# Optimization experiments

Hardware: AMD Instinct MI355X
Metric: run time of the kernel (lower is better)

## Reference

```python
import jax, jax.numpy as jnp
import numpy as np

T_VID = 129  # TACoS iou grid size

def make_iou_mask_map():
    m = np.zeros((129, 129), np.float32)
    for i in range(0, 128):
        m[i, 1 + i:min(i + 17, 129)] = 1.0
    for i in range(0, 128 - 16, 2):
        m[i, list(range(18 + i, min(33 + i, 129), 2))] = 1.0
    for i in range(0, 128 - 32, 4):
        m[i, list(range(36 + i, min(65 + i, 129), 4))] = 1.0
    for i in range(0, 128 - 64, 8):
        m[i, list(range(72 + i, 129, 8))] = 1.0
    return jnp.asarray(m)

def setup_inputs() -> dict:
    key = jax.random.key(0)
    B, L, T, D, CH, V = 8, 100, T_VID, 512, 512, 1000
    ks = jax.random.split(key, 20)
    g = lambda k, shp, fan: jax.random.normal(k, shp, jnp.float32) * (1.0 / np.sqrt(fan))
    return {
        'hidden_states_text': jax.random.normal(ks[0], (B, L, D), jnp.float32),
        'hidden_states_object': jax.random.normal(ks[1], (B, T, D), jnp.float32),
        # final_mlp (text head): D->CH->V
        'w_t1': g(ks[2], (D, CH), D), 'b_t1': jnp.zeros((CH,), jnp.float32),
        'w_t2': g(ks[3], (CH, V), CH), 'b_t2': jnp.zeros((V,), jnp.float32),
        # final_mlp_2: D -> 3D (+ReLU)
        'w2': g(ks[4], (D, 3 * D), D), 'b2': jnp.zeros((3 * D,), jnp.float32),
        # final_mlp_3: 3D -> CH -> 3
        'w3a': g(ks[5], (3 * D, CH), 3 * D), 'b3a': jnp.zeros((CH,), jnp.float32),
        'w3b': g(ks[6], (CH, 3), CH), 'b3b': jnp.zeros((3,), jnp.float32),
        # final_mlp_s/e/c: D -> CH -> 1
        'w_s1': g(ks[7], (D, CH), D), 'b_s1': jnp.zeros((CH,), jnp.float32),
        'w_s2': g(ks[8], (CH, 1), CH), 'b_s2': jnp.zeros((1,), jnp.float32),
        'w_e1': g(ks[9], (D, CH), D), 'b_e1': jnp.zeros((CH,), jnp.float32),
        'w_e2': g(ks[10], (CH, 1), CH), 'b_e2': jnp.zeros((1,), jnp.float32),
        'w_c1': g(ks[11], (D, CH), D), 'b_c1': jnp.zeros((CH,), jnp.float32),
        'w_c2': g(ks[12], (CH, 1), CH), 'b_c2': jnp.zeros((1,), jnp.float32),
    }

def _head(x, w1, b1, w2, b2):
    return jax.nn.relu(x @ w1 + b1) @ w2 + b2

def reference(hidden_states_text, hidden_states_object,
              w_t1, b_t1, w_t2, b_t2, w2, b2, w3a, b3a, w3b, b3b,
              w_s1, b_s1, w_s2, b_s2, w_e1, b_e1, w_e2, b_e2,
              w_c1, b_c1, w_c2, b_c2):
    D = hidden_states_object.shape[-1]
    T = hidden_states_object.shape[1]
    # text head (dropout is identity at inference)
    logits_text = _head(hidden_states_text, w_t1, b_t1, w_t2, b_t2)
    # final_mlp_2 then split into start/center/end streams, each [B,T,D]
    h = jax.nn.relu(hidden_states_object @ w2 + b2)
    hs, hc, he = h[..., :D], h[..., D:2 * D], h[..., 2 * D:]
    # final_mlp_3 first linear decomposed over the concat blocks:
    # grid[b,i,j] = W_s.hs[i] + W_c.hc[(i+j)//2] + W_e.he[j] + b  (same math as
    # cat(repeat(hs), gather(hc), repeat(he)) @ w3a, without the 3D grid)
    ps = hc @ w3a[D:2 * D]            # [B,T,CH] (center projection, gathered below)
    pS = hs @ w3a[:D]                 # [B,T,CH]
    pE = he @ w3a[2 * D:]             # [B,T,CH]
    idx = (jnp.arange(T)[:, None] + jnp.arange(T)[None, :]) // 2  # [T,T] center index
    grid = pS[:, :, None, :] + ps[:, idx, :] + pE[:, None, :, :] + b3a  # [B,T,T,CH]
    logits_iou = (jax.nn.relu(grid) @ w3b + b3b)  # [B,T,T,3]
    logits_iou = jnp.transpose(logits_iou, (0, 3, 1, 2))  # [B,3,T,T]
    logits_visual = jnp.concatenate([
        _head(hs, w_s1, b_s1, w_s2, b_s2),
        _head(he, w_e1, b_e1, w_e2, b_e2),
        _head(hc, w_c1, b_c1, w_c2, b_c2)], axis=-1)  # [B,T,3]
    return logits_text, logits_visual, logits_iou, make_iou_mask_map()
```

## Files before the change

### kernel.cpp

```cpp
#include <hip/hip_runtime.h>
#include <hip/hip_bf16.h>

typedef unsigned short ushort_t;
typedef __attribute__((ext_vector_type(8))) short bf16x8;
typedef __attribute__((ext_vector_type(4))) float f32x4;

constexpr int BB = 8, LL = 100, TT = 129, DD = 512, CH = 512, VV = 1000;
constexpr int M_TXT = BB * LL;
constexpr int M_OBJ = BB * TT;
constexpr int P_SLAB = M_OBJ * DD;
constexpr int N_IOU = BB * 3 * TT * TT;
constexpr int N_VIS = 3 * M_OBJ;
constexpr int N_MASK = TT * TT;

constexpr int OUT_TEXT = 0;
constexpr int OUT_VIS  = M_TXT * VV;
constexpr int OUT_IOU  = OUT_VIS + N_VIS;
constexpr int OUT_MASK = OUT_IOU + N_IOU;

constexpr size_t WB_TEXT = 0;
constexpr size_t WB_OBJ  = WB_TEXT + 819200;
constexpr size_t WB_WT1  = WB_OBJ  + 1056768;
constexpr size_t WB_WT2  = WB_WT1  + 524288;
constexpr size_t WB_W2T  = WB_WT2  + 1024000;
constexpr size_t WB_W3AT = WB_W2T  + 1572864;
constexpr size_t WB_WS1T = WB_W3AT + 1572864;
constexpr size_t WB_WE1T = WB_WS1T + 524288;
constexpr size_t WB_WC1T = WB_WE1T + 524288;
constexpr size_t WB_T1   = WB_WC1T + 524288;
constexpr size_t WB_H    = WB_T1   + 819200;
constexpr size_t WB_P    = WB_H    + 3170304;

__device__ __forceinline__ ushort_t f2bf(float x) {
    __hip_bfloat16 h = __float2bfloat16(x);
    return *(ushort_t*)&h;
}

struct TDesc { const float* src; ushort_t* dst; int R, C, tiles, ctiles; };
struct PrepArgs {
    const float* act_a; ushort_t* act_da; int na4;
    const float* act_b; ushort_t* act_db; int nb4;
    int nact_blocks, nwt_blocks;
    TDesc t[7];
    const float *b3b, *bs2, *be2, *bc2;
    float* out;
};

__global__ __launch_bounds__(256)
void prep_kernel(PrepArgs pa)
{
    const int bxg = blockIdx.x;
    if (bxg < pa.nact_blocks) {
        int gid = bxg * 256 + threadIdx.x;
        const float* src; ushort_t* dst;
        if (gid < pa.na4) { src = pa.act_a + gid * 4; dst = pa.act_da + gid * 4; }
        else { gid -= pa.na4; if (gid >= pa.nb4) return; src = pa.act_b + gid * 4; dst = pa.act_db + gid * 4; }
        f32x4 v = *(const f32x4*)src;
        dst[0] = f2bf(v[0]); dst[1] = f2bf(v[1]); dst[2] = f2bf(v[2]); dst[3] = f2bf(v[3]);
        return;
    }
    if (bxg < pa.nact_blocks + pa.nwt_blocks) {
        __shared__ float tl[32][33];
        int bx = bxg - pa.nact_blocks;
        TDesc e;
        #pragma unroll
        for (int i = 0; i < 7; ++i) {
            if (bx < pa.t[i].tiles) { e = pa.t[i]; break; }
            bx -= pa.t[i].tiles;
        }
        const int tx = threadIdx.x & 31, ty = threadIdx.x >> 5;
        const int rt = bx / e.ctiles, ct = bx - rt * e.ctiles;
        #pragma unroll
        for (int i = 0; i < 4; ++i) {
            const int r = rt * 32 + ty + i * 8, c = ct * 32 + tx;
            tl[ty + i * 8][tx] = (r < e.R && c < e.C) ? e.src[(size_t)r * e.C + c] : 0.0f;
        }
        __syncthreads();
        #pragma unroll
        for (int i = 0; i < 4; ++i) {
            const int dr = ct * 32 + ty + i * 8, dc = rt * 32 + tx;
            if (dr < e.C && dc < e.R)
                e.dst[(size_t)dr * e.R + dc] = f2bf(tl[tx][ty + i * 8]);
        }
        return;
    }
    int g = (bxg - pa.nact_blocks - pa.nwt_blocks) * 256 + threadIdx.x;
    if (g < N_IOU) {
        const int bk = g / (TT * TT);
        const int k = bk - (bk / 3) * 3;
        pa.out[OUT_IOU + g] = pa.b3b[k];
        return;
    }
    g -= N_IOU;
    if (g < N_VIS) {
        const int head = g - (g / 3) * 3;
        const float bias = head == 0 ? pa.bs2[0] : (head == 1 ? pa.be2[0] : pa.bc2[0]);
        pa.out[OUT_VIS + g] = bias;
        return;
    }
    g -= N_VIS;
    if (g < N_MASK) {
        const int i = g / TT, j = g - i * TT;
        const int d = j - i;
        bool v = false;
        if (i < 128 && d >= 1 && d <= 16) v = true;
        if (!v && (i & 1) == 0 && i <= 110 && d >= 18 && d <= 32 && (d & 1) == 0) v = true;
        if (!v && (i & 3) == 0 && i <= 92  && d >= 36 && d <= 64 && (d & 3) == 0) v = true;
        if (!v && (i & 7) == 0 && i <= 56  && d >= 72 && (d & 7) == 0) v = true;
        pa.out[OUT_MASK + g] = v ? 1.0f : 0.0f;
    }
}

struct GemmDesc {
    const ushort_t* A; int lda;
    const ushort_t* Bt; int ldb;
    const float* bias;
    void* C; int ldc;
    int M, N, K;
    int mode;
    const float* w2head;
    float* vbase;
    int vhead;
    int ntiles, ntx;
};
struct GemmArgs { GemmDesc d[7]; };

__global__ __launch_bounds__(256)
void gemm_mfma(GemmArgs args)
{
    int bx = blockIdx.x, zi = 0;
    while (bx >= args.d[zi].ntiles) { bx -= args.d[zi].ntiles; ++zi; }
    const GemmDesc g = args.d[zi];
    const int tyT = bx / g.ntx, txT = bx - tyT * g.ntx;
    const int m0 = tyT * 128, n0 = txT * 128;

    __shared__ ushort_t ldsA[2][128 * 32];
    __shared__ ushort_t ldsB[2][128 * 32];

    const int tid = threadIdx.x;
    const int w = tid >> 6, l = tid & 63;
    const int wr = w >> 1, wc = w & 1;

    const int srow = l >> 2;
    const int scol = (l & 3) << 3;
    const int wbase = w << 4;

    f32x4 acc[4][4];
    #pragma unroll
    for (int mi = 0; mi < 4; ++mi)
        #pragma unroll
        for (int ni = 0; ni < 4; ++ni)
            acc[mi][ni] = f32x4{0.f, 0.f, 0.f, 0.f};

    const int nk = g.K >> 5;

    auto stage = [&](int buf, int k0) {
        #pragma unroll
        for (int q = 0; q < 2; ++q) {
            int gm = m0 + (q << 6) + wbase + srow; if (gm >= g.M) gm = g.M - 1;
            __builtin_amdgcn_global_load_lds(
                (const __attribute__((address_space(1))) unsigned int*)(g.A + (size_t)gm * g.lda + k0 + scol),
                (__attribute__((address_space(3))) unsigned int*)&ldsA[buf][((q << 6) + wbase) * 32],
                16, 0, 0);
            int gn = n0 + (q << 6) + wbase + srow; if (gn >= g.N) gn = g.N - 1;
            __builtin_amdgcn_global_load_lds(
                (const __attribute__((address_space(1))) unsigned int*)(g.Bt + (size_t)gn * g.ldb + k0 + scol),
                (__attribute__((address_space(3))) unsigned int*)&ldsB[buf][((q << 6) + wbase) * 32],
                16, 0, 0);
        }
    };

    stage(0, 0);
    int cur = 0;
    const int fr = l & 15, kq = (l >> 4) << 3;

    for (int kt = 0; kt < nk; ++kt) {
        __syncthreads();
        if (kt + 1 < nk) stage(cur ^ 1, (kt + 1) << 5);
        bf16x8 av[4], bv[4];
        #pragma unroll
        for (int mi = 0; mi < 4; ++mi)
            av[mi] = *(const bf16x8*)&ldsA[cur][((wr << 6) + (mi << 4) + fr) * 32 + kq];
        #pragma unroll
        for (int ni = 0; ni < 4; ++ni)
            bv[ni] = *(const bf16x8*)&ldsB[cur][((wc << 6) + (ni << 4) + fr) * 32 + kq];
        #pragma unroll
        for (int mi = 0; mi < 4; ++mi)
            #pragma unroll
            for (int ni = 0; ni < 4; ++ni)
                acc[mi][ni] = __builtin_amdgcn_mfma_f32_16x16x32_bf16(av[mi], bv[ni], acc[mi][ni], 0, 0, 0);
        cur ^= 1;
    }

    const int rq = (l >> 4) << 2;
    if (g.mode == 2) {
        float s[4][4];
        #pragma unroll
        for (int mi = 0; mi < 4; ++mi)
            #pragma unroll
            for (int r = 0; r < 4; ++r) s[mi][r] = 0.f;
        #pragma unroll
        for (int ni = 0; ni < 4; ++ni) {
            const int col = n0 + (wc << 6) + (ni << 4) + fr;
            const float bb = g.bias[col];
            const float wv = g.w2head[col];
            #pragma unroll
            for (int mi = 0; mi < 4; ++mi)
                #pragma unroll
                for (int r = 0; r < 4; ++r) {
                    float v = fmaxf(acc[mi][ni][r] + bb, 0.f);
                    s[mi][r] = fmaf(v, wv, s[mi][r]);
                }
        }
        #pragma unroll
        for (int off = 1; off < 16; off <<= 1)
            #pragma unroll
            for (int mi = 0; mi < 4; ++mi)
                #pragma unroll
                for (int r = 0; r < 4; ++r)
                    s[mi][r] += __shfl_xor(s[mi][r], off);
        if (fr == 0) {
            #pragma unroll
            for (int mi = 0; mi < 4; ++mi)
                #pragma unroll
                for (int r = 0; r < 4; ++r) {
                    const int row = m0 + (wr << 6) + (mi << 4) + rq + r;
                    if (row < g.M) atomicAdd(&g.vbase[row * 3 + g.vhead], s[mi][r]);
                }
        }
    } else {
        #pragma unroll
        for (int ni = 0; ni < 4; ++ni) {
            const int col = n0 + (wc << 6) + (ni << 4) + fr;
            const float bb = (g.bias && col < g.N) ? g.bias[col] : 0.f;
            #pragma unroll
            for (int mi = 0; mi < 4; ++mi)
                #pragma unroll
                for (int r = 0; r < 4; ++r) {
                    const int row = m0 + (wr << 6) + (mi << 4) + rq + r;
                    if (row < g.M && col < g.N) {
                        float v = acc[mi][ni][r] + bb;
                        if (g.mode == 1) {
                            v = fmaxf(v, 0.f);
                            ((ushort_t*)g.C)[(size_t)row * g.ldc + col] = f2bf(v);
                        } else {
                            ((float*)g.C)[(size_t)row * g.ldc + col] = v;
                        }
                    }
                }
        }
    }
}

__global__ __launch_bounds__(256)
void iou_kernel(const float* __restrict__ P, const float* __restrict__ w3b,
                float* __restrict__ out)
{
    __shared__ __align__(16) float sP[96 * 132];
    __shared__ __align__(16) float sW[384];

    const int tid = threadIdx.x;
    const int b = blockIdx.z >> 2;
    const int cs = blockIdx.z & 3;
    const int c0 = cs << 7;
    const int i0 = blockIdx.y * 32, j0 = blockIdx.x * 32;
    const int idx0 = (i0 + j0) >> 1;
    const int par = (i0 + j0) & 1;

    for (int f = tid; f < 384; f += 256) {
        const int k = f >> 7, c = f & 127;
        sW[f] = w3b[(c0 + c) * 3 + k];
    }
    for (int f = tid; f < 3072; f += 256) {
        const int row = f >> 5;
        const int pos = (f & 31) << 2;
        const int a = row >> 5;
        const int r = row & 31;
        int rg = (a == 0) ? (i0 + r) : (a == 1) ? (idx0 + r) : (j0 + r);
        if (rg > 128) rg = 128;
        f32x4 v = *(const f32x4*)&P[(size_t)a * P_SLAB + ((size_t)(b * TT) + rg) * DD + c0 + pos];
        *(f32x4*)&sP[row * 132 + pos] = v;
    }
    __syncthreads();

    const int ii = tid >> 4, jj = tid & 15;
    const int o = ((ii + jj + par) >> 1) + 32;

    const float* rs0 = &sP[ii * 132];
    const float* rs1 = &sP[(ii + 16) * 132];
    const float* rp0 = &sP[o * 132];
    const float* rp1 = &sP[(o + 8) * 132];
    const float* rp2 = &sP[(o + 16) * 132];
    const float* re0 = &sP[(64 + jj) * 132];
    const float* re1 = &sP[(64 + jj + 16) * 132];

    const f32x4 z4 = {0.f, 0.f, 0.f, 0.f};
    f32x4 av00[3], av01[3], av10[3], av11[3];
    #pragma unroll
    for (int k = 0; k < 3; ++k) { av00[k] = z4; av01[k] = z4; av10[k] = z4; av11[k] = z4; }

    #pragma unroll 2
    for (int c = 0; c < 128; c += 4) {
        const f32x4 s0 = *(const f32x4*)&rs0[c];
        const f32x4 s1 = *(const f32x4*)&rs1[c];
        const f32x4 p0 = *(const f32x4*)&rp0[c];
        const f32x4 p1 = *(const f32x4*)&rp1[c];
        const f32x4 p2 = *(const f32x4*)&rp2[c];
        const f32x4 e0 = *(const f32x4*)&re0[c];
        const f32x4 e1 = *(const f32x4*)&re1[c];
        const f32x4 w0 = *(const f32x4*)&sW[c];
        const f32x4 w1 = *(const f32x4*)&sW[128 + c];
        const f32x4 w2 = *(const f32x4*)&sW[256 + c];

        const f32x4 t00 = s0 + e0, t01 = s0 + e1, t10 = s1 + e0, t11 = s1 + e1;
        const f32x4 v00 = __builtin_elementwise_max(t00 + p0, z4);
        const f32x4 v01 = __builtin_elementwise_max(t01 + p1, z4);
        const f32x4 v10 = __builtin_elementwise_max(t10 + p1, z4);
        const f32x4 v11 = __builtin_elementwise_max(t11 + p2, z4);

        av00[0] = __builtin_elementwise_fma(v00, w0, av00[0]);
        av00[1] = __builtin_elementwise_fma(v00, w1, av00[1]);
        av00[2] = __builtin_elementwise_fma(v00, w2, av00[2]);
        av01[0] = __builtin_elementwise_fma(v01, w0, av01[0]);
        av01[1] = __builtin_elementwise_fma(v01, w1, av01[1]);
        av01[2] = __builtin_elementwise_fma(v01, w2, av01[2]);
        av10[0] = __builtin_elementwise_fma(v10, w0, av10[0]);
        av10[1] = __builtin_elementwise_fma(v10, w1, av10[1]);
        av10[2] = __builtin_elementwise_fma(v10, w2, av10[2]);
        av11[0] = __builtin_elementwise_fma(v11, w0, av11[0]);
        av11[1] = __builtin_elementwise_fma(v11, w1, av11[1]);
        av11[2] = __builtin_elementwise_fma(v11, w2, av11[2]);
    }

    auto emit = [&](const f32x4* acc, int i, int j) {
        if (i <= 128 && j <= 128) {
            #pragma unroll
            for (int k = 0; k < 3; ++k) {
                const float s = acc[k][0] + acc[k][1] + acc[k][2] + acc[k][3];
                atomicAdd(&out[OUT_IOU + ((size_t)(b * 3 + k) * TT + i) * TT + j], s);
            }
        }
    };
    emit(av00, i0 + ii, j0 + jj);
    emit(av01, i0 + ii, j0 + jj + 16);
    emit(av10, i0 + ii + 16, j0 + jj);
    emit(av11, i0 + ii + 16, j0 + jj + 16);
}

extern "C" void kernel_launch(void* const* d_in, const int* in_sizes, int n_in,
                              void* d_out, int out_size, void* d_ws, size_t ws_size,
                              hipStream_t stream)
{
    const float* text = (const float*)d_in[0];
    const float* obj  = (const float*)d_in[1];
    const float* w_t1 = (const float*)d_in[2];
    const float* b_t1 = (const float*)d_in[3];
    const float* w_t2 = (const float*)d_in[4];
    const float* b_t2 = (const float*)d_in[5];
    const float* w2   = (const float*)d_in[6];
    const float* b2   = (const float*)d_in[7];
    const float* w3a  = (const float*)d_in[8];
    const float* b3a  = (const float*)d_in[9];
    const float* w3b  = (const float*)d_in[10];
    const float* b3b  = (const float*)d_in[11];
    const float* w_s1 = (const float*)d_in[12];
    const float* b_s1 = (const float*)d_in[13];
    const float* w_s2 = (const float*)d_in[14];
    const float* b_s2 = (const float*)d_in[15];
    const float* w_e1 = (const float*)d_in[16];
    const float* b_e1 = (const float*)d_in[17];
    const float* w_e2 = (const float*)d_in[18];
    const float* b_e2 = (const float*)d_in[19];
    const float* w_c1 = (const float*)d_in[20];
    const float* b_c1 = (const float*)d_in[21];
    const float* w_c2 = (const float*)d_in[22];
    const float* b_c2 = (const float*)d_in[23];

    float* out = (float*)d_out;
    char* ws = (char*)d_ws;
    ushort_t* text_bf = (ushort_t*)(ws + WB_TEXT);
    ushort_t* obj_bf  = (ushort_t*)(ws + WB_OBJ);
    ushort_t* wt1     = (ushort_t*)(ws + WB_WT1);
    ushort_t* wt2     = (ushort_t*)(ws + WB_WT2);
    ushort_t* w2t     = (ushort_t*)(ws + WB_W2T);
    ushort_t* w3at    = (ushort_t*)(ws + WB_W3AT);
    ushort_t* ws1t    = (ushort_t*)(ws + WB_WS1T);
    ushort_t* we1t    = (ushort_t*)(ws + WB_WE1T);
    ushort_t* wc1t    = (ushort_t*)(ws + WB_WC1T);
    ushort_t* T1      = (ushort_t*)(ws + WB_T1);
    ushort_t* H       = (ushort_t*)(ws + WB_H);
    float*    P       = (float*)(ws + WB_P);

    {
        PrepArgs pa;
        pa.act_a = text; pa.act_da = text_bf; pa.na4 = (M_TXT * DD) / 4;
        pa.act_b = obj;  pa.act_db = obj_bf;  pa.nb4 = (M_OBJ * DD) / 4;
        pa.nact_blocks = (pa.na4 + pa.nb4 + 255) / 256;
        pa.nwt_blocks = 3072;
        pa.t[0] = {w_t1, wt1, 512, 512, 256, 16};
        pa.t[1] = {w_t2, wt2, 512, 1000, 512, 32};
        pa.t[2] = {w2, w2t, 512, 1536, 768, 48};
        pa.t[3] = {w3a, w3at, 1536, 512, 768, 16};
        pa.t[4] = {w_s1, ws1t, 512, 512, 256, 16};
        pa.t[5] = {w_e1, we1t, 512, 512, 256, 16};
        pa.t[6] = {w_c1, wc1t, 512, 512, 256, 16};
        pa.b3b = b3b; pa.bs2 = b_s2; pa.be2 = b_e2; pa.bc2 = b_c2;
        pa.out = out;
        const int ninit = (N_IOU + N_VIS + N_MASK + 255) / 256;
        prep_kernel<<<dim3(pa.nact_blocks + pa.nwt_blocks + ninit), dim3(256), 0, stream>>>(pa);
    }
    {
        GemmArgs a{};
        a.d[0] = {text_bf, DD, wt1, DD, b_t1, T1, CH, M_TXT, CH, DD, 1, nullptr, nullptr, 0, 28, 4};
        a.d[1] = {obj_bf, DD, w2t, DD, b2, H, 3 * DD, M_OBJ, 3 * DD, DD, 1, nullptr, nullptr, 0, 108, 12};
        gemm_mfma<<<dim3(136), dim3(256), 0, stream>>>(a);
    }
    {
        GemmArgs a{};
        a.d[0] = {T1, CH, wt2, CH, b_t2, out + OUT_TEXT, VV, M_TXT, VV, CH, 0, nullptr, nullptr, 0, 56, 8};
        a.d[1] = {H + 0 * DD, 3 * DD, w3at + 0 * DD, 3 * DD, b3a, P + 0 * P_SLAB, DD, M_OBJ, DD, DD, 0, nullptr, nullptr, 0, 36, 4};
        a.d[2] = {H + 1 * DD, 3 * DD, w3at + 1 * DD, 3 * DD, nullptr, P + 1 * P_SLAB, DD, M_OBJ, DD, DD, 0, nullptr, nullptr, 0, 36, 4};
        a.d[3] = {H + 2 * DD, 3 * DD, w3at + 2 * DD, 3 * DD, nullptr, P + 2 * P_SLAB, DD, M_OBJ, DD, DD, 0, nullptr, nullptr, 0, 36, 4};
        a.d[4] = {H + 0 * DD, 3 * DD, ws1t, DD, b_s1, nullptr, 0, M_OBJ, CH, DD, 2, w_s2, out + OUT_VIS, 0, 36, 4};
        a.d[5] = {H + 2 * DD, 3 * DD, we1t, DD, b_e1, nullptr, 0, M_OBJ, CH, DD, 2, w_e2, out + OUT_VIS, 1, 36, 4};
        a.d[6] = {H + 1 * DD, 3 * DD, wc1t, DD, b_c1, nullptr, 0, M_OBJ, CH, DD, 2, w_c2, out + OUT_VIS, 2, 36, 4};
        gemm_mfma<<<dim3(272), dim3(256), 0, stream>>>(a);
    }
    iou_kernel<<<dim3(5, 5, 32), dim3(256), 0, stream>>>(P, w3b, out);
}
```

Baseline: 87.46 us.

## Vectorize transpose stores, deepen GEMM K-step to 64, halve IoU atomic splits

The weight-transpose path now writes four bf16 values per thread in one packed store instead of scattered scalar stores. The MFMA GEMM stages 64 K-elements per barrier, doubling LDS buffers, to halve the number of sync iterations. The IoU kernel makes each block loop over two 128-channel chunks, halving grid size and atomicAdd traffic at the cost of less parallelism and serialized loads. The transpose store assumes the column range is full 32-wide and aligned with no dc<R check, which could write out of bounds or drop the tail when R is not a multiple of 32.

Result: faster. 81.86 us (-6.4%).

```diff
diff --git a/kernel.cpp b/kernel.cpp
--- a/kernel.cpp
+++ b/kernel.cpp
@@ -2,6 +2,7 @@
 #include <hip/hip_bf16.h>
 
 typedef unsigned short ushort_t;
+typedef __attribute__((ext_vector_type(4))) unsigned short u16x4;
 typedef __attribute__((ext_vector_type(8))) short bf16x8;
 typedef __attribute__((ext_vector_type(4))) float f32x4;
 
@@ -68,7 +69,8 @@
             if (bx < pa.t[i].tiles) { e = pa.t[i]; break; }
             bx -= pa.t[i].tiles;
         }
-        const int tx = threadIdx.x & 31, ty = threadIdx.x >> 5;
+        const int t = threadIdx.x;
+        const int tx = t & 31, ty = t >> 5;
         const int rt = bx / e.ctiles, ct = bx - rt * e.ctiles;
         #pragma unroll
         for (int i = 0; i < 4; ++i) {
@@ -76,11 +78,13 @@
             tl[ty + i * 8][tx] = (r < e.R && c < e.C) ? e.src[(size_t)r * e.C + c] : 0.0f;
         }
         __syncthreads();
-        #pragma unroll
-        for (int i = 0; i < 4; ++i) {
-            const int dr = ct * 32 + ty + i * 8, dc = rt * 32 + tx;
-            if (dr < e.C && dc < e.R)
-                e.dst[(size_t)dr * e.R + dc] = f2bf(tl[tx][ty + i * 8]);
+        const int drl = t >> 3, dcl = (t & 7) << 2;
+        const int grow = ct * 32 + drl;
+        if (grow < e.C) {
+            u16x4 v;
+            #pragma unroll
+            for (int u = 0; u < 4; ++u) v[u] = f2bf(tl[dcl + u][drl]);
+            *(u16x4*)&e.dst[(size_t)grow * e.R + rt * 32 + dcl] = v;
         }
         return;
     }
@@ -134,8 +138,8 @@
     const int tyT = bx / g.ntx, txT = bx - tyT * g.ntx;
     const int m0 = tyT * 128, n0 = txT * 128;
 
-    __shared__ ushort_t ldsA[2][128 * 32];
-    __shared__ ushort_t ldsB[2][128 * 32];
+    __shared__ ushort_t ldsA[2][2][128 * 32];
+    __shared__ ushort_t ldsB[2][2][128 * 32];
 
     const int tid = threadIdx.x;
     const int w = tid >> 6, l = tid & 63;
@@ -152,21 +156,24 @@
         for (int ni = 0; ni < 4; ++ni)
             acc[mi][ni] = f32x4{0.f, 0.f, 0.f, 0.f};
 
-    const int nk = g.K >> 5;
+    const int nk = g.K >> 6;
 
     auto stage = [&](int buf, int k0) {
         #pragma unroll
-        for (int q = 0; q < 2; ++q) {
-            int gm = m0 + (q << 6) + wbase + srow; if (gm >= g.M) gm = g.M - 1;
-            __builtin_amdgcn_global_load_lds(
-                (const __attribute__((address_space(1))) unsigned int*)(g.A + (size_t)gm * g.lda + k0 + scol),
-                (__attribute__((address_space(3))) unsigned int*)&ldsA[buf][((q << 6) + wbase) * 32],
-                16, 0, 0);
-            int gn = n0 + (q << 6) + wbase + srow; if (gn >= g.N) gn = g.N - 1;
-            __builtin_amdgcn_global_load_lds(
-                (const __attribute__((address_space(1))) unsigned int*)(g.Bt + (size_t)gn * g.ldb + k0 + scol),
-                (__attribute__((address_space(3))) unsigned int*)&ldsB[buf][((q << 6) + wbase) * 32],
-                16, 0, 0);
+        for (int ks = 0; ks < 2; ++ks) {
+            #pragma unroll
+            for (int q = 0; q < 2; ++q) {
+                int gm = m0 + (q << 6) + wbase + srow; if (gm >= g.M) gm = g.M - 1;
+                __builtin_amdgcn_global_load_lds(
+                    (const __attribute__((address_space(1))) unsigned int*)(g.A + (size_t)gm * g.lda + k0 + (ks << 5) + scol),
+                    (__attribute__((address_space(3))) unsigned int*)&ldsA[buf][ks][((q << 6) + wbase) * 32],
+                    16, 0, 0);
+                int gn = n0 + (q << 6) + wbase + srow; if (gn >= g.N) gn = g.N - 1;
+                __builtin_amdgcn_global_load_lds(
+                    (const __attribute__((address_space(1))) unsigned int*)(g.Bt + (size_t)gn * g.ldb + k0 + (ks << 5) + scol),
+                    (__attribute__((address_space(3))) unsigned int*)&ldsB[buf][ks][((q << 6) + wbase) * 32],
+                    16, 0, 0);
+            }
         }
     };
 
@@ -176,19 +183,22 @@
 
     for (int kt = 0; kt < nk; ++kt) {
         __syncthreads();
-        if (kt + 1 < nk) stage(cur ^ 1, (kt + 1) << 5);
-        bf16x8 av[4], bv[4];
-        #pragma unroll
-        for (int mi = 0; mi < 4; ++mi)
-            av[mi] = *(const bf16x8*)&ldsA[cur][((wr << 6) + (mi << 4) + fr) * 32 + kq];
-        #pragma unroll
-        for (int ni = 0; ni < 4; ++ni)
-            bv[ni] = *(const bf16x8*)&ldsB[cur][((wc << 6) + (ni << 4) + fr) * 32 + kq];
-        #pragma unroll
-        for (int mi = 0; mi < 4; ++mi)
+        if (kt + 1 < nk) stage(cur ^ 1, (kt + 1) << 6);
+        #pragma unroll
+        for (int ks = 0; ks < 2; ++ks) {
+            bf16x8 av[4], bv[4];
+            #pragma unroll
+            for (int mi = 0; mi < 4; ++mi)
+                av[mi] = *(const bf16x8*)&ldsA[cur][ks][((wr << 6) + (mi << 4) + fr) * 32 + kq];
             #pragma unroll
             for (int ni = 0; ni < 4; ++ni)
-                acc[mi][ni] = __builtin_amdgcn_mfma_f32_16x16x32_bf16(av[mi], bv[ni], acc[mi][ni], 0, 0, 0);
+                bv[ni] = *(const bf16x8*)&ldsB[cur][ks][((wc << 6) + (ni << 4) + fr) * 32 + kq];
+            #pragma unroll
+            for (int mi = 0; mi < 4; ++mi)
+                #pragma unroll
+                for (int ni = 0; ni < 4; ++ni)
+                    acc[mi][ni] = __builtin_amdgcn_mfma_f32_16x16x32_bf16(av[mi], bv[ni], acc[mi][ni], 0, 0, 0);
+        }
         cur ^= 1;
     }
 
@@ -260,76 +270,79 @@
     __shared__ __align__(16) float sW[384];
 
     const int tid = threadIdx.x;
-    const int b = blockIdx.z >> 2;
-    const int cs = blockIdx.z & 3;
-    const int c0 = cs << 7;
+    const int b = blockIdx.z >> 1;
+    const int half = blockIdx.z & 1;
     const int i0 = blockIdx.y * 32, j0 = blockIdx.x * 32;
     const int idx0 = (i0 + j0) >> 1;
     const int par = (i0 + j0) & 1;
 
-    for (int f = tid; f < 384; f += 256) {
-        const int k = f >> 7, c = f & 127;
-        sW[f] = w3b[(c0 + c) * 3 + k];
-    }
-    for (int f = tid; f < 3072; f += 256) {
-        const int row = f >> 5;
-        const int pos = (f & 31) << 2;
-        const int a = row >> 5;
-        const int r = row & 31;
-        int rg = (a == 0) ? (i0 + r) : (a == 1) ? (idx0 + r) : (j0 + r);
-        if (rg > 128) rg = 128;
-        f32x4 v = *(const f32x4*)&P[(size_t)a * P_SLAB + ((size_t)(b * TT) + rg) * DD + c0 + pos];
-        *(f32x4*)&sP[row * 132 + pos] = v;
-    }
-    __syncthreads();
-
     const int ii = tid >> 4, jj = tid & 15;
     const int o = ((ii + jj + par) >> 1) + 32;
-
-    const float* rs0 = &sP[ii * 132];
-    const float* rs1 = &sP[(ii + 16) * 132];
-    const float* rp0 = &sP[o * 132];
-    const float* rp1 = &sP[(o + 8) * 132];
-    const float* rp2 = &sP[(o + 16) * 132];
-    const float* re0 = &sP[(64 + jj) * 132];
-    const float* re1 = &sP[(64 + jj + 16) * 132];
 
     const f32x4 z4 = {0.f, 0.f, 0.f, 0.f};
     f32x4 av00[3], av01[3], av10[3], av11[3];
     #pragma unroll
     for (int k = 0; k < 3; ++k) { av00[k] = z4; av01[k] = z4; av10[k] = z4; av11[k] = z4; }
 
-    #pragma unroll 2
-    for (int c = 0; c < 128; c += 4) {
-        const f32x4 s0 = *(const f32x4*)&rs0[c];
-        const f32x4 s1 = *(const f32x4*)&rs1[c];
-        const f32x4 p0 = *(const f32x4*)&rp0[c];
-        const f32x4 p1 = *(const f32x4*)&rp1[c];
-        const f32x4 p2 = *(const f32x4*)&rp2[c];
-        const f32x4 e0 = *(const f32x4*)&re0[c];
-        const f32x4 e1 = *(const f32x4*)&re1[c];
-        const f32x4 w0 = *(const f32x4*)&sW[c];
-        const f32x4 w1 = *(const f32x4*)&sW[128 + c];
-        const f32x4 w2 = *(const f32x4*)&sW[256 + c];
-
-        const f32x4 t00 = s0 + e0, t01 = s0 + e1, t10 = s1 + e0, t11 = s1 + e1;
-        const f32x4 v00 = __builtin_elementwise_max(t00 + p0, z4);
-        const f32x4 v01 = __builtin_elementwise_max(t01 + p1, z4);
-        const f32x4 v10 = __builtin_elementwise_max(t10 + p1, z4);
-        const f32x4 v11 = __builtin_elementwise_max(t11 + p2, z4);
-
-        av00[0] = __builtin_elementwise_fma(v00, w0, av00[0]);
-        av00[1] = __builtin_elementwise_fma(v00, w1, av00[1]);
-        av00[2] = __builtin_elementwise_fma(v00, w2, av00[2]);
-        av01[0] = __builtin_elementwise_fma(v01, w0, av01[0]);
-        av01[1] = __builtin_elementwise_fma(v01, w1, av01[1]);
-        av01[2] = __builtin_elementwise_fma(v01, w2, av01[2]);
-        av10[0] = __builtin_elementwise_fma(v10, w0, av10[0]);
-        av10[1] = __builtin_elementwise_fma(v10, w1, av10[1]);
-        av10[2] = __builtin_elementwise_fma(v10, w2, av10[2]);
-        av11[0] = __builtin_elementwise_fma(v11, w0, av11[0]);
-        av11[1] = __builtin_elementwise_fma(v11, w1, av11[1]);
-        av11[2] = __builtin_elementwise_fma(v11, w2, av11[2]);
+    for (int ph = 0; ph < 2; ++ph) {
+        const int c0 = (half << 8) + (ph << 7);
+        if (ph) __syncthreads();
+        for (int f = tid; f < 384; f += 256) {
+            const int k = f >> 7, c = f & 127;
+            sW[f] = w3b[(c0 + c) * 3 + k];
+        }
+        for (int f = tid; f < 3072; f += 256) {
+            const int row = f >> 5;
+            const int pos = (f & 31) << 2;
+            const int a = row >> 5;
+            const int r = row & 31;
+            int rg = (a == 0) ? (i0 + r) : (a == 1) ? (idx0 + r) : (j0 + r);
+            if (rg > 128) rg = 128;
+            f32x4 v = *(const f32x4*)&P[(size_t)a * P_SLAB + ((size_t)(b * TT) + rg) * DD + c0 + pos];
+            *(f32x4*)&sP[row * 132 + pos] = v;
+        }
+        __syncthreads();
+
+        const float* rs0 = &sP[ii * 132];
+        const float* rs1 = &sP[(ii + 16) * 132];
+        const float* rp0 = &sP[o * 132];
+        const float* rp1 = &sP[(o + 8) * 132];
+        const float* rp2 = &sP[(o + 16) * 132];
+        const float* re0 = &sP[(64 + jj) * 132];
+        const float* re1 = &sP[(64 + jj + 16) * 132];
+
+        #pragma unroll 2
+        for (int c = 0; c < 128; c += 4) {
+            const f32x4 s0 = *(const f32x4*)&rs0[c];
+            const f32x4 s1 = *(const f32x4*)&rs1[c];
+            const f32x4 p0 = *(const f32x4*)&rp0[c];
+            const f32x4 p1 = *(const f32x4*)&rp1[c];
+            const f32x4 p2 = *(const f32x4*)&rp2[c];
+            const f32x4 e0 = *(const f32x4*)&re0[c];
+            const f32x4 e1 = *(const f32x4*)&re1[c];
+            const f32x4 w0 = *(const f32x4*)&sW[c];
+            const f32x4 w1 = *(const f32x4*)&sW[128 + c];
+            const f32x4 w2 = *(const f32x4*)&sW[256 + c];
+
+            const f32x4 t00 = s0 + e0, t01 = s0 + e1, t10 = s1 + e0, t11 = s1 + e1;
+            const f32x4 v00 = __builtin_elementwise_max(t00 + p0, z4);
+            const f32x4 v01 = __builtin_elementwise_max(t01 + p1, z4);
+            const f32x4 v10 = __builtin_elementwise_max(t10 + p1, z4);
+            const f32x4 v11 = __builtin_elementwise_max(t11 + p2, z4);
+
+            av00[0] = __builtin_elementwise_fma(v00, w0, av00[0]);
+            av00[1] = __builtin_elementwise_fma(v00, w1, av00[1]);
+            av00[2] = __builtin_elementwise_fma(v00, w2, av00[2]);
+            av01[0] = __builtin_elementwise_fma(v01, w0, av01[0]);
+            av01[1] = __builtin_elementwise_fma(v01, w1, av01[1]);
+            av01[2] = __builtin_elementwise_fma(v01, w2, av01[2]);
+            av10[0] = __builtin_elementwise_fma(v10, w0, av10[0]);
+            av10[1] = __builtin_elementwise_fma(v10, w1, av10[1]);
+            av10[2] = __builtin_elementwise_fma(v10, w2, av10[2]);
+            av11[0] = __builtin_elementwise_fma(v11, w0, av11[0]);
+            av11[1] = __builtin_elementwise_fma(v11, w1, av11[1]);
+            av11[2] = __builtin_elementwise_fma(v11, w2, av11[2]);
+        }
     }
 
     auto emit = [&](const f32x4* acc, int i, int j) {
@@ -426,5 +439,5 @@
         a.d[6] = {H + 1 * DD, 3 * DD, wc1t, DD, b_c1, nullptr, 0, M_OBJ, CH, DD, 2, w_c2, out + OUT_VIS, 2, 36, 4};
         gemm_mfma<<<dim3(272), dim3(256), 0, stream>>>(a);
     }
-    iou_kernel<<<dim3(5, 5, 32), dim3(256), 0, stream>>>(P, w3b, out);
+    iou_kernel<<<dim3(5, 5, 16), dim3(256), 0, stream>>>(P, w3b, out);
 }
```
